# Optimization experiments

Measured on AMD Instinct MI355X. Metric: run time of the kernel, lower is better.

## Reference

```python
import jax, jax.numpy as jnp
import numpy as np

N = 10000
E = 640000
D_IN = 128
D_OUT = 128


def setup_inputs() -> dict:
    key = jax.random.key(0)
    k_x, k_e, k_w, k_b = jax.random.split(key, 4)
    x = jax.random.normal(k_x, (N, D_IN), dtype=jnp.float32)
    edge_index = jax.random.randint(k_e, (2, E), 0, N, dtype=jnp.int64)
    # nn.Linear params (PyTorch stores weight as [out, in]; we keep [in, out])
    fc_w = jax.random.normal(k_w, (D_IN, D_OUT), dtype=jnp.float32) / np.sqrt(D_IN)
    fc_b = jax.random.normal(k_b, (D_OUT,), dtype=jnp.float32) * 0.01
    # LayerNorm affine params
    ln_w = jnp.ones((D_OUT,), dtype=jnp.float32)
    ln_b = jnp.zeros((D_OUT,), dtype=jnp.float32)
    return {"x": x, "edge_index": edge_index, "fc_w": fc_w, "fc_b": fc_b,
            "ln_w": ln_w, "ln_b": ln_b}


def _layer_norm(h, w, b, eps=1e-5):
    mu = jnp.mean(h, axis=-1, keepdims=True)
    var = jnp.var(h, axis=-1, keepdims=True)
    return (h - mu) * jax.lax.rsqrt(var + eps) * w + b


def reference(x, edge_index, fc_w, fc_b, ln_w, ln_b):
    # Linear transform: [N, D_OUT]
    h = x @ fc_w + fc_b
    # Per-edge scatter-add: x_agg[dst] += h[src]  (self term included: agg starts at h)
    src, dst = edge_index[0], edge_index[1]
    agg = h + jax.ops.segment_sum(h[src], dst, num_segments=N)
    # LayerNorm then ReLU
    return jax.nn.relu(_layer_norm(agg, ln_w, ln_b))
```

## Files before the change

kernel.cpp:

```cpp
#include <hip/hip_runtime.h>

#define NN 10000
#define NE 640000
#define D  128
#define CAP 128
#define CSTRIDE 16


__device__ __forceinline__ float2 bf2f(unsigned u) {
  float2 r;
  r.x = __uint_as_float(u << 16);
  r.y = __uint_as_float(u & 0xffff0000u);
  return r;
}

__global__ __launch_bounds__(128) void gemm_kernel(
    const float* __restrict__ x, const float* __restrict__ W,
    const float* __restrict__ b, unsigned short* __restrict__ hb) {
  __shared__ float xs[16 * D];
  const int tid  = threadIdx.x;
  const int row0 = blockIdx.x * 16;
  #pragma unroll
  for (int r = 0; r < 16; ++r)
    xs[r * D + tid] = x[(row0 + r) * D + tid];
  __syncthreads();
  float acc[16];
  #pragma unroll
  for (int r = 0; r < 16; ++r) acc[r] = 0.f;
  for (int i = 0; i < D; i += 4) {
    const float w0 = W[(i + 0) * D + tid];
    const float w1 = W[(i + 1) * D + tid];
    const float w2 = W[(i + 2) * D + tid];
    const float w3 = W[(i + 3) * D + tid];
    #pragma unroll
    for (int r = 0; r < 16; ++r) {
      const float4 xv = *(const float4*)(&xs[r * D + i]);
      float a = acc[r];
      a = fmaf(xv.x, w0, a);
      a = fmaf(xv.y, w1, a);
      a = fmaf(xv.z, w2, a);
      a = fmaf(xv.w, w3, a);
      acc[r] = a;
    }
  }
  const float bias = b[tid];
  #pragma unroll
  for (int r = 0; r < 16; ++r) {
    const float v = acc[r] + bias;
    unsigned uv = __float_as_uint(v);
    uv += 0x7fffu + ((uv >> 16) & 1u);
    hb[(row0 + r) * D + tid] = (unsigned short)(uv >> 16);
  }
}

__global__ __launch_bounds__(256) void place_kernel(const int* __restrict__ ei,
                                                    int* __restrict__ cnt,
                                                    int* __restrict__ bucket) {
  const int base_e = blockIdx.x * 1024 + threadIdx.x;
  int src[4], dst[4], pos[4];
  #pragma unroll
  for (int i = 0; i < 4; ++i) {
    const int e = base_e + i * 256;
    src[i] = ei[e];
    dst[i] = ei[NE + e];
  }
  #pragma unroll
  for (int i = 0; i < 4; ++i)
    pos[i] = atomicAdd(&cnt[dst[i] * CSTRIDE], 1);
  #pragma unroll
  for (int i = 0; i < 4; ++i)
    if (pos[i] < CAP)
      bucket[dst[i] * CAP + pos[i]] = src[i];
}

__global__ __launch_bounds__(256) void gather_ln_kernel(
    const unsigned short* __restrict__ hb, const int* __restrict__ cnt,
    const int* __restrict__ bucket, const float* __restrict__ lw,
    const float* __restrict__ lb, float* __restrict__ out) {
  const int tid  = threadIdx.x;
  const int node = blockIdx.x * 4 + (tid >> 6);
  const int l16  = tid & 15;
  const int sel  = (tid >> 4) & 3;
  const uint4* __restrict__ h4 = (const uint4*)hb;

  float acc[8];
  #pragma unroll
  for (int j = 0; j < 8; ++j) acc[j] = 0.f;

  #define ACC16(v)  do {                         \
    float2 p0 = bf2f((v).x), p1 = bf2f((v).y);   \
    float2 p2 = bf2f((v).z), p3 = bf2f((v).w);   \
    acc[0] += p0.x; acc[1] += p0.y;              \
    acc[2] += p1.x; acc[3] += p1.y;              \
    acc[4] += p2.x; acc[5] += p2.y;              \
    acc[6] += p3.x; acc[7] += p3.y; } while (0)

  if (sel == 0) {
    const uint4 v = h4[node * 16 + l16];
    ACC16(v);
  }

  int n = cnt[node * CSTRIDE];
  if (n > CAP) n = CAP;
  const int base = node * CAP;
  int e = 0;
  for (; e + 16 <= n; e += 16) {
    const int s0 = bucket[base + e + 0  + sel];
    const int s1 = bucket[base + e + 4  + sel];
    const int s2 = bucket[base + e + 8  + sel];
    const int s3 = bucket[base + e + 12 + sel];
    const uint4 v0 = h4[s0 * 16 + l16];
    const uint4 v1 = h4[s1 * 16 + l16];
    const uint4 v2 = h4[s2 * 16 + l16];
    const uint4 v3 = h4[s3 * 16 + l16];
    ACC16(v0); ACC16(v1); ACC16(v2); ACC16(v3);
  }
  for (; e + 4 <= n; e += 4) {
    const uint4 v = h4[bucket[base + e + sel] * 16 + l16];
    ACC16(v);
  }
  const int rem = n - e;
  if (sel < rem) {
    const uint4 v = h4[bucket[base + e + sel] * 16 + l16];
    ACC16(v);
  }
  #undef ACC16

  #pragma unroll
  for (int j = 0; j < 8; ++j) {
    acc[j] += __shfl_xor(acc[j], 16);
    acc[j] += __shfl_xor(acc[j], 32);
  }

  float s = 0.f, q = 0.f;
  #pragma unroll
  for (int j = 0; j < 8; ++j) { s += acc[j]; q += acc[j] * acc[j]; }
  #pragma unroll
  for (int off = 8; off; off >>= 1) {
    s += __shfl_xor(s, off);
    q += __shfl_xor(q, off);
  }
  const float mean = s * (1.f / 128.f);
  const float var  = q * (1.f / 128.f) - mean * mean;
  const float rstd = rsqrtf(var + 1e-5f);

  if (sel == 0) {
    const int c = l16 * 8;
    const float4 wa = *(const float4*)(lw + c);
    const float4 wb = *(const float4*)(lw + c + 4);
    const float4 ba = *(const float4*)(lb + c);
    const float4 bb = *(const float4*)(lb + c + 4);
    float4 y0, y1;
    y0.x = fmaxf((acc[0] - mean) * rstd * wa.x + ba.x, 0.f);
    y0.y = fmaxf((acc[1] - mean) * rstd * wa.y + ba.y, 0.f);
    y0.z = fmaxf((acc[2] - mean) * rstd * wa.z + ba.z, 0.f);
    y0.w = fmaxf((acc[3] - mean) * rstd * wa.w + ba.w, 0.f);
    y1.x = fmaxf((acc[4] - mean) * rstd * wb.x + bb.x, 0.f);
    y1.y = fmaxf((acc[5] - mean) * rstd * wb.y + bb.y, 0.f);
    y1.z = fmaxf((acc[6] - mean) * rstd * wb.z + bb.z, 0.f);
    y1.w = fmaxf((acc[7] - mean) * rstd * wb.w + bb.w, 0.f);
    *(float4*)(out + node * D + c)     = y0;
    *(float4*)(out + node * D + c + 4) = y1;
  }
}

extern "C" void kernel_launch(void* const* d_in, const int* in_sizes, int n_in,
                              void* d_out, int out_size, void* d_ws, size_t ws_size,
                              hipStream_t stream) {
  const float* x  = (const float*)d_in[0];
  const int*   ei = (const int*)  d_in[1];
  const float* fw = (const float*)d_in[2];
  const float* fb = (const float*)d_in[3];
  const float* lw = (const float*)d_in[4];
  const float* lb = (const float*)d_in[5];
  float* out = (float*)d_out;

  char* ws = (char*)d_ws;
  unsigned short* hb = (unsigned short*)ws;  ws += (size_t)NN * D * sizeof(unsigned short);
  int* cnt = (int*)ws;                       ws += (size_t)NN * CSTRIDE * sizeof(int);
  int* bucket = (int*)ws;

  hipMemsetAsync(cnt, 0, (size_t)NN * CSTRIDE * sizeof(int), stream);
  gemm_kernel     <<<NN / 16, 128, 0, stream>>>(x, fw, fb, hb);
  place_kernel    <<<NE / 1024, 256, 0, stream>>>(ei, cnt, bucket);
  gather_ln_kernel<<<NN / 4, 256, 0, stream>>>(hb, cnt, bucket, lw, lb, out);
}
```

Baseline: 129.5 us.

## Fuse GEMM and edge-bucketing kernels into one interleaved launch

Combines the linear-transform GEMM and the edge placement (atomic bucketing) kernels into a single launch. Even blocks compute the GEMM and odd blocks place edges, so the compute-bound and atomic-bound phases can run at the same time and one launch is removed. GEMM blocks now use 256 threads, each handling 8 rows instead of 16. The cost is some divergence in register and shared memory needs between the two block roles, and shared memory is allocated even for placement blocks.

```diff
diff --git a/kernel.cpp b/kernel.cpp
--- a/kernel.cpp
+++ b/kernel.cpp
@@ -14,63 +14,69 @@
   return r;
 }
 
-__global__ __launch_bounds__(128) void gemm_kernel(
+__global__ __launch_bounds__(256) void fused_gemm_place_kernel(
     const float* __restrict__ x, const float* __restrict__ W,
-    const float* __restrict__ b, unsigned short* __restrict__ hb) {
+    const float* __restrict__ b, unsigned short* __restrict__ hb,
+    const int* __restrict__ ei, int* __restrict__ cnt,
+    int* __restrict__ bucket) {
   __shared__ float xs[16 * D];
-  const int tid  = threadIdx.x;
-  const int row0 = blockIdx.x * 16;
-  #pragma unroll
-  for (int r = 0; r < 16; ++r)
-    xs[r * D + tid] = x[(row0 + r) * D + tid];
-  __syncthreads();
-  float acc[16];
-  #pragma unroll
-  for (int r = 0; r < 16; ++r) acc[r] = 0.f;
-  for (int i = 0; i < D; i += 4) {
-    const float w0 = W[(i + 0) * D + tid];
-    const float w1 = W[(i + 1) * D + tid];
-    const float w2 = W[(i + 2) * D + tid];
-    const float w3 = W[(i + 3) * D + tid];
+  if ((blockIdx.x & 1) == 0) {
+    const int blk  = blockIdx.x >> 1;
+    const int tid  = threadIdx.x;
+    const int f    = tid & 127;
+    const int rg   = tid >> 7;
+    const int row0 = blk * 16;
     #pragma unroll
-    for (int r = 0; r < 16; ++r) {
-      const float4 xv = *(const float4*)(&xs[r * D + i]);
-      float a = acc[r];
-      a = fmaf(xv.x, w0, a);
-      a = fmaf(xv.y, w1, a);
-      a = fmaf(xv.z, w2, a);
-      a = fmaf(xv.w, w3, a);
-      acc[r] = a;
+    for (int k = 0; k < 8; ++k) {
+      const int idx = k * 256 + tid;
+      xs[idx] = x[row0 * D + idx];
     }
+    __syncthreads();
+    float acc[8];
+    #pragma unroll
+    for (int r = 0; r < 8; ++r) acc[r] = 0.f;
+    for (int i = 0; i < D; i += 4) {
+      const float w0 = W[(i + 0) * D + f];
+      const float w1 = W[(i + 1) * D + f];
+      const float w2 = W[(i + 2) * D + f];
+      const float w3 = W[(i + 3) * D + f];
+      #pragma unroll
+      for (int r = 0; r < 8; ++r) {
+        const float4 xv = *(const float4*)(&xs[(rg * 8 + r) * D + i]);
+        float a = acc[r];
+        a = fmaf(xv.x, w0, a);
+        a = fmaf(xv.y, w1, a);
+        a = fmaf(xv.z, w2, a);
+        a = fmaf(xv.w, w3, a);
+        acc[r] = a;
+      }
+    }
+    const float bias = b[f];
+    #pragma unroll
+    for (int r = 0; r < 8; ++r) {
+      const float v = acc[r] + bias;
+      unsigned uv = __float_as_uint(v);
+      uv += 0x7fffu + ((uv >> 16) & 1u);
+      hb[(row0 + rg * 8 + r) * D + f] = (unsigned short)(uv >> 16);
+    }
+  } else {
+    const int pb = blockIdx.x >> 1;
+    const int base_e = pb * 1024 + threadIdx.x;
+    int src[4], dst[4], pos[4];
+    #pragma unroll
+    for (int i = 0; i < 4; ++i) {
+      const int e = base_e + i * 256;
+      src[i] = ei[e];
+      dst[i] = ei[NE + e];
+    }
+    #pragma unroll
+    for (int i = 0; i < 4; ++i)
+      pos[i] = atomicAdd(&cnt[dst[i] * CSTRIDE], 1);
+    #pragma unroll
+    for (int i = 0; i < 4; ++i)
+      if (pos[i] < CAP)
+        bucket[dst[i] * CAP + pos[i]] = src[i];
   }
-  const float bias = b[tid];
-  #pragma unroll
-  for (int r = 0; r < 16; ++r) {
-    const float v = acc[r] + bias;
-    unsigned uv = __float_as_uint(v);
-    uv += 0x7fffu + ((uv >> 16) & 1u);
-    hb[(row0 + r) * D + tid] = (unsigned short)(uv >> 16);
-  }
-}
-
-__global__ __launch_bounds__(256) void place_kernel(const int* __restrict__ ei,
-                                                    int* __restrict__ cnt,
-                                                    int* __restrict__ bucket) {
-  const int base_e = blockIdx.x * 1024 + threadIdx.x;
-  int src[4], dst[4], pos[4];
-  #pragma unroll
-  for (int i = 0; i < 4; ++i) {
-    const int e = base_e + i * 256;
-    src[i] = ei[e];
-    dst[i] = ei[NE + e];
-  }
-  #pragma unroll
-  for (int i = 0; i < 4; ++i)
-    pos[i] = atomicAdd(&cnt[dst[i] * CSTRIDE], 1);
-  #pragma unroll
-  for (int i = 0; i < 4; ++i)
-    if (pos[i] < CAP)
-      bucket[dst[i] * CAP + pos[i]] = src[i];
 }
 
 __global__ __launch_bounds__(256) void gather_ln_kernel(
@@ -181,7 +187,6 @@
   int* bucket = (int*)ws;
 
   hipMemsetAsync(cnt, 0, (size_t)NN * CSTRIDE * sizeof(int), stream);
-  gemm_kernel     <<<NN / 16, 128, 0, stream>>>(x, fw, fb, hb);
-  place_kernel    <<<NE / 1024, 256, 0, stream>>>(ei, cnt, bucket);
-  gather_ln_kernel<<<NN / 4, 256, 0, stream>>>(hb, cnt, bucket, lw, lb, out);
+  fused_gemm_place_kernel<<<1250, 256, 0, stream>>>(x, fw, fb, hb, ei, cnt, bucket);
+  gather_ln_kernel       <<<NN / 4, 256, 0, stream>>>(hb, cnt, bucket, lw, lb, out);
 }
```

Result: faster. 115.6 us (-10.7%).
